# Kernel optimization log

Measured on AMD Instinct MI355X. Metric: run time of the kernel, lower is better.

Reference implementation:

```python
import jax, jax.numpy as jnp
import numpy as np

N_NODES = 100000
N_EDGES = 6_400_000
IN_DIM = 128


def gcn_conv(x, W, b, row, col, ew):
    """PyG GCNConv(normalize=True, add_self_loops=True) forward."""
    n = x.shape[0]
    loop = jnp.arange(n)
    row_sl = jnp.concatenate([row, loop])
    col_sl = jnp.concatenate([col, loop])
    ew_sl = jnp.concatenate([ew, jnp.ones((n,), ew.dtype)])
    # symmetric normalization: deg^{-1/2}[src] * w * deg^{-1/2}[dst]
    deg = jax.ops.segment_sum(ew_sl, col_sl, num_segments=n)
    safe_deg = jnp.where(deg > 0, deg, 1.0)
    dis = jnp.where(deg > 0, jax.lax.rsqrt(safe_deg), 0.0)
    norm = dis[row_sl] * ew_sl * dis[col_sl]
    h = x @ W  # [n, out_dim] linear transform first (small out_dim)
    # gather source features, scale, scatter-add into targets
    out = jax.ops.segment_sum(norm[:, None] * h[row_sl], col_sl, num_segments=n)
    return out + b


def setup_inputs() -> dict:
    key = jax.random.key(0)
    ks = jax.random.split(key, 12)
    X = jax.random.normal(ks[0], (N_NODES, IN_DIM), dtype=jnp.float32)
    edge_index = jax.random.randint(ks[1], (2, N_EDGES), 0, N_NODES, dtype=jnp.int64)
    edge_weight = jax.random.uniform(ks[2], (N_EDGES,), dtype=jnp.float32)

    def glorot(k, fan_in, fan_out):
        lim = np.sqrt(6.0 / (fan_in + fan_out)).astype(np.float32)
        return jax.random.uniform(k, (fan_in, fan_out), minval=-lim, maxval=lim, dtype=jnp.float32)

    return {
        "X": X,
        "edge_index": edge_index,
        "edge_weight": edge_weight,
        "W1": glorot(ks[3], IN_DIM, 12), "b1": jnp.zeros((12,), jnp.float32),
        "W2": glorot(ks[4], 12, 6), "b2": jnp.zeros((6,), jnp.float32),
        "W3": glorot(ks[5], 6, 3), "b3": jnp.zeros((3,), jnp.float32),
        "Wl": glorot(ks[6], 3, 1), "bl": jnp.zeros((1,), jnp.float32),
    }


def reference(X, edge_index, edge_weight, W1, b1, W2, b2, W3, b3, Wl, bl):
    row, col = edge_index[0], edge_index[1]
    h = jax.nn.relu(gcn_conv(X, W1, b1, row, col, edge_weight))
    # dropout p=0.2 is identity in eval mode
    h = jax.nn.relu(gcn_conv(h, W2, b2, row, col, edge_weight))
    h = jax.nn.relu(gcn_conv(h, W3, b3, row, col, edge_weight))
    out = jax.nn.sigmoid(h @ Wl + bl)
    return out.squeeze(1)  # [N]
```

## Files before the change

### kernel.cpp

```cpp
#include <hip/hip_runtime.h>
#include <cstdint>
#include <cstddef>

#define RANGE    128
#define RSHIFT   7
#define MAXBUCK  800
#define CSHIFT   12
#define CRANGE   4096
#define MAXC     32
#define FPB      32
#define CH_CNT   8192
#define CH_SC    4096
#define EPT      16
#define PAD      16
#define WSTR     132
#define STAGE_CAP 9216
#define KMAX     18

typedef _Float16 h8 __attribute__((ext_vector_type(8)));

__global__ void zero_pad_kernel(int* __restrict__ p, int n) {
    int i = blockIdx.x * blockDim.x + threadIdx.x;
    if (i < n) p[i * PAD] = 0;
}

__global__ void count_kernel(const int* __restrict__ col, int* __restrict__ fcnt,
                             int nfine, int E) {
    __shared__ int lcnt[MAXBUCK];
    int tid = threadIdx.x;
    for (int i = tid; i < nfine; i += blockDim.x) lcnt[i] = 0;
    __syncthreads();
    int base = blockIdx.x * CH_CNT;
    int end  = min(E, base + CH_CNT);
    for (int e = base + tid; e < end; e += blockDim.x)
        atomicAdd(&lcnt[col[e] >> RSHIFT], 1);
    __syncthreads();
    for (int i = tid; i < nfine; i += blockDim.x)
        if (lcnt[i]) atomicAdd(&fcnt[i * PAD], lcnt[i]);
}

__global__ void scan_kernel(const int* __restrict__ fcnt, int* __restrict__ fbase,
                            int* __restrict__ fcur, int* __restrict__ cbase,
                            int* __restrict__ ccur, int* __restrict__ row_ptr,
                            int nfine, int ncoarse, int N, int E) {
    __shared__ int lds[1024];
    int T = threadIdx.x;
    int s = (T < nfine) ? fcnt[T * PAD] : 0;
    lds[T] = s;
    __syncthreads();
    for (int off = 1; off < 1024; off <<= 1) {
        int v = (T >= off) ? lds[T - off] : 0;
        __syncthreads();
        lds[T] += v;
        __syncthreads();
    }
    int excl = lds[T] - s;
    if (T < nfine) { fbase[T] = excl; fcur[T * PAD] = excl; }
    if ((T & (FPB - 1)) == 0 && (T >> 5) < ncoarse) {
        cbase[T >> 5] = excl;
        ccur[(T >> 5) * PAD] = excl;
    }
    if (T == 0) { fbase[nfine] = E; cbase[ncoarse] = E; row_ptr[N] = E; }
}

__global__ void coarse_scatter_kernel(const int* __restrict__ row, const int* __restrict__ col,
                                      const float* __restrict__ ew, int* __restrict__ ccur,
                                      uint2* __restrict__ partA, int ncoarse, int E) {
    __shared__ uint2 stage[CH_SC];
    __shared__ unsigned char sb[CH_SC];
    __shared__ int lcnt[MAXC], lofs[MAXC], gofs[MAXC];
    __shared__ int total_s;
    int tid = threadIdx.x;
    if (tid < MAXC) lcnt[tid] = 0;
    __syncthreads();
    int base = blockIdx.x * CH_SC;
    int cnt  = min(E - base, CH_SC);

    uint2 rec[EPT]; int rnk[EPT]; int bb[EPT];
#pragma unroll
    for (int k = 0; k < EPT; k++) {
        int idx = tid + (k << 8);
        if (idx < cnt) {
            int e = base + idx;
            int c = col[e];
            int b = c >> CSHIFT;
            bb[k]  = b;
            rec[k] = make_uint2((unsigned)row[e] | ((unsigned)(c & (CRANGE - 1)) << 17),
                                __float_as_uint(ew[e]));
            rnk[k] = atomicAdd(&lcnt[b], 1);
        }
    }
    __syncthreads();
    if (tid == 0) {
        int run = 0;
        for (int i = 0; i < ncoarse; i++) { lofs[i] = run; run += lcnt[i]; }
        total_s = run;
    }
    __syncthreads();
    if (tid < ncoarse) {
        int c = lcnt[tid];
        if (c) {
            int g = atomicAdd(&ccur[tid * PAD], c);
            gofs[tid] = g - lofs[tid];
        }
    }
#pragma unroll
    for (int k = 0; k < EPT; k++) {
        int idx = tid + (k << 8);
        if (idx < cnt) {
            int p = lofs[bb[k]] + rnk[k];
            stage[p] = rec[k];
            sb[p] = (unsigned char)bb[k];
        }
    }
    __syncthreads();
    int total = total_s;
    for (int i = tid; i < total; i += 256)
        partA[gofs[sb[i]] + i] = stage[i];
}

__global__ __launch_bounds__(256, 3)
void fine_scatter_kernel(const uint2* __restrict__ partA, const int* __restrict__ cbase,
                                    int* __restrict__ fcur, uint2* __restrict__ partB,
                                    int nfine, int ncoarse, int E) {
    __shared__ uint2 stage[CH_SC];
    __shared__ unsigned short sb[CH_SC];
    __shared__ int lcnt[MAXBUCK], lofs[MAXBUCK], gofs[MAXBUCK];
    __shared__ int tmp[256];
    __shared__ int scb[MAXC + 1];
    __shared__ int rlo_s, total_s;
    int tid = threadIdx.x;
    int base = blockIdx.x * CH_SC;
    int cnt  = min(E - base, CH_SC);
    if (tid <= ncoarse) scb[tid] = cbase[tid];
    for (int i = tid; i < nfine; i += 256) lcnt[i] = 0;
    if (tid == 0) {
        int r = 0;
        while (r < ncoarse - 1 && cbase[r + 1] <= base) ++r;
        rlo_s = r;
    }
    __syncthreads();
    int rlo = rlo_s;

    uint2 rec[EPT]; int rnk[EPT]; int ff[EPT];
#pragma unroll
    for (int k = 0; k < EPT; k++) {
        int idx = tid + (k << 8);
        if (idx < cnt) {
            int e = base + idx;
            uint2 v = partA[e];
            int r = rlo;
            while (e >= scb[r + 1]) ++r;
            int col12 = (int)((v.x >> 17) & (CRANGE - 1));
            int f = (r << 5) | (col12 >> RSHIFT);
            ff[k]  = f;
            rec[k] = make_uint2((v.x & 0x1FFFFu) | ((unsigned)(col12 & (RANGE - 1)) << 17), v.y);
            rnk[k] = atomicAdd(&lcnt[f], 1);
        }
    }
    __syncthreads();
    {
        const int Cc = (nfine + 255) >> 8;
        int b0 = tid * Cc;
        int s = 0;
        for (int i = 0; i < Cc; i++) {
            int idx = b0 + i;
            if (idx < nfine) s += lcnt[idx];
        }
        tmp[tid] = s;
        __syncthreads();
        for (int off = 1; off < 256; off <<= 1) {
            int v = (tid >= off) ? tmp[tid - off] : 0;
            __syncthreads();
            tmp[tid] += v;
            __syncthreads();
        }
        int run = tmp[tid] - s;
        for (int i = 0; i < Cc; i++) {
            int idx = b0 + i;
            if (idx < nfine) { lofs[idx] = run; run += lcnt[idx]; }
        }
        if (tid == 255) total_s = tmp[255];
    }
    __syncthreads();
    for (int i = tid; i < nfine; i += 256) {
        int c = lcnt[i];
        if (c) {
            int g = atomicAdd(&fcur[i * PAD], c);
            gofs[i] = g - lofs[i];
        }
    }
#pragma unroll
    for (int k = 0; k < EPT; k++) {
        int idx = tid + (k << 8);
        if (idx < cnt) {
            int p = lofs[ff[k]] + rnk[k];
            stage[p] = rec[k];
            sb[p] = (unsigned short)ff[k];
        }
    }
    __syncthreads();
    int total = total_s;
    for (int i = tid; i < total; i += 256)
        partB[gofs[sb[i]] + i] = stage[i];
}

__global__ __launch_bounds__(512, 4)
void bucket_csr_kernel(const uint2* __restrict__ part, const int* __restrict__ bbase,
                       int* __restrict__ row_ptr, float* __restrict__ dis,
                       uint2* __restrict__ csr, int N) {
    extern __shared__ uint2 stage[];
    __shared__ int   scnt[RANGE];
    __shared__ int   sscan[RANGE];
    __shared__ float sdeg[RANGE];
    __shared__ float sdis[RANGE];
    int b = blockIdx.x, tid = threadIdx.x;
    int s = bbase[b], t = bbase[b + 1];
    int cnt = t - s;
    if (tid < RANGE) { scnt[tid] = 0; sdeg[tid] = 1.0f; }
    __syncthreads();
    for (int idx = tid; idx < cnt; idx += 512) {
        uint2 r = part[s + idx];
        if (idx < STAGE_CAP) stage[idx] = r;
        int c = (r.x >> 17) & (RANGE - 1);
        atomicAdd(&scnt[c], 1);
        atomicAdd(&sdeg[c], __uint_as_float(r.y));
    }
    __syncthreads();
    int cnt_t = 0;
    if (tid < RANGE) { cnt_t = scnt[tid]; sscan[tid] = cnt_t; }
    __syncthreads();
    for (int off = 1; off < RANGE; off <<= 1) {
        int v = 0;
        if (tid < RANGE && tid >= off) v = sscan[tid - off];
        __syncthreads();
        if (tid < RANGE) sscan[tid] += v;
        __syncthreads();
    }
    if (tid < RANGE) {
        int excl = sscan[tid] - cnt_t;
        int node = b * RANGE + tid;
        float dn = rsqrtf(sdeg[tid]);
        sdis[tid] = dn;
        if (node < N) {
            row_ptr[node] = s + excl;
            dis[node] = dn;
        }
        scnt[tid] = excl;
    }
    __syncthreads();

    if (cnt <= STAGE_CAP) {
        uint2 rc[KMAX]; int rp[KMAX];
#pragma unroll
        for (int k = 0; k < KMAX; k++) {
            int idx = tid + k * 512;
            if (idx < cnt) {
                uint2 r = stage[idx];
                int c   = (r.x >> 17) & (RANGE - 1);
                float v = sdis[c] * __uint_as_float(r.y);
                rp[k] = atomicAdd(&scnt[c], 1);
                rc[k] = make_uint2(r.x & 0x1FFFFu, __float_as_uint(v));
            }
        }
        __syncthreads();
#pragma unroll
        for (int k = 0; k < KMAX; k++) {
            int idx = tid + k * 512;
            if (idx < cnt) stage[rp[k]] = rc[k];
        }
        __syncthreads();
        for (int i = tid; i < cnt; i += 512)
            csr[s + i] = stage[i];
    } else {
        for (int idx = tid; idx < cnt; idx += 512) {
            uint2 r = (idx < STAGE_CAP) ? stage[idx] : part[s + idx];
            int c   = (r.x >> 17) & (RANGE - 1);
            float v = sdis[c] * __uint_as_float(r.y);
            int off = atomicAdd(&scnt[c], 1);
            csr[s + off] = make_uint2(r.x & 0x1FFFFu, __float_as_uint(v));
        }
    }
}

__global__ void lin1_kernel(const float* __restrict__ X, const float* __restrict__ W1,
                            const float* __restrict__ dis, uint4* __restrict__ t1, int n) {
    __shared__ float w1t[12 * WSTR];
    int tid = threadIdx.x;
    for (int i = tid; i < 128 * 12; i += 256) {
        int k = i / 12, o = i - k * 12;
        w1t[o * WSTR + k] = W1[i];
    }
    __syncthreads();
    int gt   = blockIdx.x * 256 + tid;
    int node = gt >> 3;
    int sub  = gt & 7;
    if (node >= n) return;

    const float4* xp = (const float4*)(X + (size_t)node * 128 + sub * 16);
    float4 x0 = xp[0], x1 = xp[1], x2 = xp[2], x3 = xp[3];

    float res[12];
#pragma unroll
    for (int o = 0; o < 12; o++) {
        const float4* wp = (const float4*)(w1t + o * WSTR + sub * 16);
        float4 w0 = wp[0], w1v = wp[1], w2 = wp[2], w3 = wp[3];
        float s;
        s  = x0.x * w0.x + x0.y * w0.y + x0.z * w0.z + x0.w * w0.w;
        s += x1.x * w1v.x + x1.y * w1v.y + x1.z * w1v.z + x1.w * w1v.w;
        s += x2.x * w2.x + x2.y * w2.y + x2.z * w2.z + x2.w * w2.w;
        s += x3.x * w3.x + x3.y * w3.y + x3.z * w3.z + x3.w * w3.w;
        res[o] = s;
    }
#pragma unroll
    for (int o = 0; o < 12; o++) {
        res[o] += __shfl_xor(res[o], 1, 64);
        res[o] += __shfl_xor(res[o], 2, 64);
        res[o] += __shfl_xor(res[o], 4, 64);
    }
    if (sub == 0) {
        h8 a, b;
#pragma unroll
        for (int o = 0; o < 8; o++) a[o] = (_Float16)res[o];
#pragma unroll
        for (int o = 0; o < 4; o++) b[o] = (_Float16)res[8 + o];
#pragma unroll
        for (int o = 4; o < 8; o++) b[o] = (_Float16)0.f;
        uint4 ua = __builtin_bit_cast(uint4, a);
        uint4 ub = __builtin_bit_cast(uint4, b);
        ub.z = __float_as_uint(dis[node]);
        ub.w = 0u;
        uint4* dst = t1 + (size_t)node * 2;
        dst[0] = ua;
        dst[1] = ub;
    }
}

template <int DIN, int ROWW, int DOUT, bool LAST>
__global__ void agg_kernel(const int* __restrict__ row_ptr, const uint2* __restrict__ csr,
                           const uint4* __restrict__ hin,
                           const float* __restrict__ b_this, const float* __restrict__ W_next,
                           const float* __restrict__ b_next, void* __restrict__ hout_v, int n) {
    int gt   = blockIdx.x * blockDim.x + threadIdx.x;
    int node = gt >> 3;
    int sub  = gt & 7;
    if (node >= n) return;
    int start = row_ptr[node];
    int end   = row_ptr[node + 1];
    float acc[DIN], acc2[DIN];
#pragma unroll
    for (int d = 0; d < DIN; d++) { acc[d] = 0.f; acc2[d] = 0.f; }

    auto body = [&](unsigned long long raw, float* a_) {
        int src    = (int)(unsigned)raw;
        float ewdd = __uint_as_float((unsigned)(raw >> 32));
        const uint4* hr = hin + (size_t)src * ROWW;
        if constexpr (DIN == 12) {
            uint4 ua = hr[0], ub = hr[1];
            float norm = ewdd * __uint_as_float(ub.z);
            h8 a = __builtin_bit_cast(h8, ua);
            h8 b = __builtin_bit_cast(h8, ub);
#pragma unroll
            for (int d = 0; d < 8; d++) a_[d] += norm * (float)a[d];
#pragma unroll
            for (int d = 0; d < 4; d++) a_[8 + d] += norm * (float)b[d];
        } else if constexpr (DIN == 6) {
            uint4 u = hr[0];
            float norm = ewdd * __uint_as_float(u.w);
            h8 a = __builtin_bit_cast(h8, u);
#pragma unroll
            for (int d = 0; d < 6; d++) a_[d] += norm * (float)a[d];
        } else {
            uint4 u = hr[0];
            float norm = ewdd * __uint_as_float(u.z);
            h8 a = __builtin_bit_cast(h8, u);
#pragma unroll
            for (int d = 0; d < 3; d++) a_[d] += norm * (float)a[d];
        }
    };

    int e = start + sub;
    for (; e + 8 < end; e += 16) {
        unsigned long long raw0 =
            __builtin_nontemporal_load((const unsigned long long*)(csr + e));
        unsigned long long raw1 =
            __builtin_nontemporal_load((const unsigned long long*)(csr + e + 8));
        body(raw0, acc);
        body(raw1, acc2);
    }
    if (e < end) {
        unsigned long long raw0 =
            __builtin_nontemporal_load((const unsigned long long*)(csr + e));
        body(raw0, acc);
    }

#pragma unroll
    for (int d = 0; d < DIN; d++) {
        acc[d] += acc2[d];
        acc[d] += __shfl_xor(acc[d], 1, 64);
        acc[d] += __shfl_xor(acc[d], 2, 64);
        acc[d] += __shfl_xor(acc[d], 4, 64);
    }

    if (sub == 0) {
        const uint4* hn = hin + (size_t)node * ROWW;
        float v[DIN];
        float dn;
        if constexpr (DIN == 12) {
            uint4 ua = hn[0], ub = hn[1];
            dn = __uint_as_float(ub.z);
            float s2 = dn * dn;
            h8 a = __builtin_bit_cast(h8, ua);
            h8 b = __builtin_bit_cast(h8, ub);
#pragma unroll
            for (int d = 0; d < 8; d++) v[d] = fmaxf(acc[d] + s2 * (float)a[d] + b_this[d], 0.f);
#pragma unroll
            for (int d = 0; d < 4; d++) v[8 + d] = fmaxf(acc[8 + d] + s2 * (float)b[d] + b_this[8 + d], 0.f);
        } else if constexpr (DIN == 6) {
            uint4 u = hn[0];
            dn = __uint_as_float(u.w);
            float s2 = dn * dn;
            h8 a = __builtin_bit_cast(h8, u);
#pragma unroll
            for (int d = 0; d < 6; d++) v[d] = fmaxf(acc[d] + s2 * (float)a[d] + b_this[d], 0.f);
        } else {
            uint4 u = hn[0];
            dn = __uint_as_float(u.z);
            float s2 = dn * dn;
            h8 a = __builtin_bit_cast(h8, u);
#pragma unroll
            for (int d = 0; d < 3; d++) v[d] = fmaxf(acc[d] + s2 * (float)a[d] + b_this[d], 0.f);
        }
        if constexpr (!LAST) {
            float o[DOUT];
#pragma unroll
            for (int oo = 0; oo < DOUT; oo++) {
                float z = 0.f;
#pragma unroll
                for (int d = 0; d < DIN; d++) z += v[d] * W_next[d * DOUT + oo];
                o[oo] = z;
            }
            h8 w;
#pragma unroll
            for (int oo = 0; oo < 8; oo++) w[oo] = (_Float16)0.f;
#pragma unroll
            for (int oo = 0; oo < DOUT; oo++) w[oo] = (_Float16)o[oo];
            uint4 uw = __builtin_bit_cast(uint4, w);
            if constexpr (DOUT == 6) uw.w = __float_as_uint(dn);
            else                     uw.z = __float_as_uint(dn);
            ((uint4*)hout_v)[node] = uw;
        } else {
            float z = b_next[0];
#pragma unroll
            for (int d = 0; d < DIN; d++) z += v[d] * W_next[d];
            ((float*)hout_v)[node] = 1.0f / (1.0f + expf(-z));
        }
    }
}

extern "C" void kernel_launch(void* const* d_in, const int* in_sizes, int n_in,
                              void* d_out, int out_size, void* d_ws, size_t ws_size,
                              hipStream_t stream) {
    const float* X  = (const float*)d_in[0];
    const int*   ei = (const int*)d_in[1];
    const float* ew = (const float*)d_in[2];
    const float* W1 = (const float*)d_in[3];
    const float* b1 = (const float*)d_in[4];
    const float* W2 = (const float*)d_in[5];
    const float* b2 = (const float*)d_in[6];
    const float* W3 = (const float*)d_in[7];
    const float* b3 = (const float*)d_in[8];
    const float* Wl = (const float*)d_in[9];
    const float* bl = (const float*)d_in[10];
    float* out = (float*)d_out;

    const int N = in_sizes[0] / 128;
    const int E = in_sizes[1] / 2;
    const int* row = ei;
    const int* col = ei + E;
    const int nfine   = (N + RANGE - 1) >> RSHIFT;
    const int ncoarse = (N + CRANGE - 1) >> CSHIFT;

    char* ws = (char*)d_ws;
    size_t off = 0;
    auto carve = [&](size_t bytes) -> void* {
        void* p = ws + off;
        off += (bytes + 255) & ~(size_t)255;
        return p;
    };
    int*   fcnt    = (int*)  carve((size_t)MAXBUCK * PAD * 4);
    int*   fcur    = (int*)  carve((size_t)MAXBUCK * PAD * 4);
    int*   ccur    = (int*)  carve((size_t)MAXC * PAD * 4);
    int*   cbase   = (int*)  carve((size_t)(MAXC + 1) * 4);
    int*   fbase   = (int*)  carve((size_t)(MAXBUCK + 1) * 4);
    int*   row_ptr = (int*)  carve((size_t)(N + 1) * 4);
    float* dis     = (float*)carve((size_t)N * 4);
    uint2* partA   = (uint2*)carve((size_t)E * 8);
    uint2* partB   = (uint2*)carve((size_t)E * 8);
    uint2* csr = partA;
    uint4* t1  = (uint4*)partB;
    uint4* t2  = t1 + (size_t)N * 2;
    uint4* t3  = t2 + (size_t)N;
    (void)ws_size; (void)n_in; (void)out_size;

    const int bCnt = (E + CH_CNT - 1) / CH_CNT;
    const int bSc  = (E + CH_SC - 1) / CH_SC;
    const int bL   = ((size_t)N * 8 + 255) / 256;
    const int bA   = ((size_t)N * 8 + 255) / 256;

    zero_pad_kernel<<<(nfine + 255) / 256, 256, 0, stream>>>(fcnt, nfine);
    count_kernel<<<bCnt, 256, 0, stream>>>(col, fcnt, nfine, E);
    scan_kernel<<<1, 1024, 0, stream>>>(fcnt, fbase, fcur, cbase, ccur, row_ptr,
                                        nfine, ncoarse, N, E);
    coarse_scatter_kernel<<<bSc, 256, 0, stream>>>(row, col, ew, ccur, partA, ncoarse, E);
    fine_scatter_kernel<<<bSc, 256, 0, stream>>>(partA, cbase, fcur, partB, nfine, ncoarse, E);
    bucket_csr_kernel<<<nfine, 512, (size_t)STAGE_CAP * sizeof(uint2), stream>>>(
        partB, fbase, row_ptr, dis, csr, N);
    lin1_kernel<<<bL, 256, 0, stream>>>(X, W1, dis, t1, N);
    agg_kernel<12, 2, 6, false><<<bA, 256, 0, stream>>>(row_ptr, csr, t1, b1, W2, nullptr, t2, N);
    agg_kernel< 6, 1, 3, false><<<bA, 256, 0, stream>>>(row_ptr, csr, t2, b2, W3, nullptr, t3, N);
    agg_kernel< 3, 1, 1, true ><<<bA, 256, 0, stream>>>(row_ptr, csr, t3, b3, Wl, bl, out, N);
}
```

Before: 515.7 us.

## Stage CSR segments into LDS via async global_load_lds in bucket and agg kernels

Uses the AMD global_load_lds builtin to copy each block's contiguous CSR/partition records straight into shared memory, in bucket_csr_kernel and in the three aggregation kernels. Each aggregation block now covers 32 nodes, loads their edge range (up to 3072 records) into LDS, then has threads read edges from LDS, falling back to global reads when the range overflows. The copies may read past the segment end, so the partB allocation is padded. This adds LDS pressure and a full wait plus barrier before compute, which may reduce occupancy and overlap.

```diff
diff --git a/kernel.cpp b/kernel.cpp
--- a/kernel.cpp
+++ b/kernel.cpp
@@ -16,8 +16,14 @@
 #define WSTR     132
 #define STAGE_CAP 9216
 #define KMAX     18
+#define SCAP     3072
 
 typedef _Float16 h8 __attribute__((ext_vector_type(8)));
+
+#define GLOAD_LDS16(gsrc, ldsb)                                                   \
+    __builtin_amdgcn_global_load_lds(                                             \
+        (const __attribute__((address_space(1))) uint32_t*)(gsrc),                \
+        (__attribute__((address_space(3))) uint32_t*)(ldsb), 16, 0, 0)
 
 __global__ void zero_pad_kernel(int* __restrict__ p, int n) {
     int i = blockIdx.x * blockDim.x + threadIdx.x;
@@ -217,11 +223,27 @@
     int b = blockIdx.x, tid = threadIdx.x;
     int s = bbase[b], t = bbase[b + 1];
     int cnt = t - s;
+    int lim = min(cnt, STAGE_CAP);
     if (tid < RANGE) { scnt[tid] = 0; sdeg[tid] = 1.0f; }
-    __syncthreads();
-    for (int idx = tid; idx < cnt; idx += 512) {
+    {
+        int wave = tid >> 6, lane = tid & 63;
+        int iters = (lim + 1023) >> 10;
+        for (int it = 0; it < iters; ++it) {
+            int recBase = (it << 10) + (wave << 7);
+            const uint2* src = part + s + recBase + (lane << 1);
+            GLOAD_LDS16(src, (char*)stage + ((size_t)recBase << 3));
+        }
+    }
+    asm volatile("s_waitcnt vmcnt(0)" ::: "memory");
+    __syncthreads();
+    for (int idx = tid; idx < lim; idx += 512) {
+        uint2 r = stage[idx];
+        int c = (r.x >> 17) & (RANGE - 1);
+        atomicAdd(&scnt[c], 1);
+        atomicAdd(&sdeg[c], __uint_as_float(r.y));
+    }
+    for (int idx = STAGE_CAP + tid; idx < cnt; idx += 512) {
         uint2 r = part[s + idx];
-        if (idx < STAGE_CAP) stage[idx] = r;
         int c = (r.x >> 17) & (RANGE - 1);
         atomicAdd(&scnt[c], 1);
         atomicAdd(&sdeg[c], __uint_as_float(r.y));
@@ -337,13 +359,33 @@
 }
 
 template <int DIN, int ROWW, int DOUT, bool LAST>
-__global__ void agg_kernel(const int* __restrict__ row_ptr, const uint2* __restrict__ csr,
-                           const uint4* __restrict__ hin,
-                           const float* __restrict__ b_this, const float* __restrict__ W_next,
-                           const float* __restrict__ b_next, void* __restrict__ hout_v, int n) {
-    int gt   = blockIdx.x * blockDim.x + threadIdx.x;
-    int node = gt >> 3;
-    int sub  = gt & 7;
+__global__ __launch_bounds__(256)
+void agg_kernel(const int* __restrict__ row_ptr, const uint2* __restrict__ csr,
+                const uint4* __restrict__ hin,
+                const float* __restrict__ b_this, const float* __restrict__ W_next,
+                const float* __restrict__ b_next, void* __restrict__ hout_v, int n) {
+    __shared__ uint2 scsr[SCAP];
+    int tid = threadIdx.x;
+    int nodeBase = blockIdx.x << 5;
+    int node = nodeBase + (tid >> 3);
+    int sub  = tid & 7;
+    int endNode  = min(nodeBase + 32, n);
+    int blkStart = row_ptr[nodeBase];
+    int blkEnd   = row_ptr[endNode];
+    int blkCnt   = blkEnd - blkStart;
+    int lim = min(blkCnt, SCAP);
+    {
+        int wave = tid >> 6, lane = tid & 63;
+        int iters = (lim + 511) >> 9;
+        for (int it = 0; it < iters; ++it) {
+            int recBase = (it << 9) + (wave << 7);
+            const uint2* src = csr + blkStart + recBase + (lane << 1);
+            GLOAD_LDS16(src, (char*)scsr + ((size_t)recBase << 3));
+        }
+    }
+    asm volatile("s_waitcnt vmcnt(0)" ::: "memory");
+    __syncthreads();
+
     if (node >= n) return;
     int start = row_ptr[node];
     int end   = row_ptr[node + 1];
@@ -351,9 +393,9 @@
 #pragma unroll
     for (int d = 0; d < DIN; d++) { acc[d] = 0.f; acc2[d] = 0.f; }
 
-    auto body = [&](unsigned long long raw, float* a_) {
-        int src    = (int)(unsigned)raw;
-        float ewdd = __uint_as_float((unsigned)(raw >> 32));
+    auto body = [&](uint2 r, float* a_) {
+        int src    = (int)(r.x);
+        float ewdd = __uint_as_float(r.y);
         const uint4* hr = hin + (size_t)src * ROWW;
         if constexpr (DIN == 12) {
             uint4 ua = hr[0], ub = hr[1];
@@ -379,19 +421,26 @@
         }
     };
 
-    int e = start + sub;
-    for (; e + 8 < end; e += 16) {
-        unsigned long long raw0 =
-            __builtin_nontemporal_load((const unsigned long long*)(csr + e));
-        unsigned long long raw1 =
-            __builtin_nontemporal_load((const unsigned long long*)(csr + e + 8));
-        body(raw0, acc);
-        body(raw1, acc2);
-    }
-    if (e < end) {
-        unsigned long long raw0 =
-            __builtin_nontemporal_load((const unsigned long long*)(csr + e));
-        body(raw0, acc);
+    if (blkCnt <= SCAP) {
+        int ls = start - blkStart;
+        int le = end - blkStart;
+        int e = ls + sub;
+        for (; e + 8 < le; e += 16) {
+            uint2 r0 = scsr[e];
+            uint2 r1 = scsr[e + 8];
+            body(r0, acc);
+            body(r1, acc2);
+        }
+        if (e < le) body(scsr[e], acc);
+    } else {
+        int e = start + sub;
+        for (; e + 8 < end; e += 16) {
+            uint2 r0 = csr[e];
+            uint2 r1 = csr[e + 8];
+            body(r0, acc);
+            body(r1, acc2);
+        }
+        if (e < end) body(csr[e], acc);
     }
 
 #pragma unroll
@@ -496,7 +545,7 @@
     int*   row_ptr = (int*)  carve((size_t)(N + 1) * 4);
     float* dis     = (float*)carve((size_t)N * 4);
     uint2* partA   = (uint2*)carve((size_t)E * 8);
-    uint2* partB   = (uint2*)carve((size_t)E * 8);
+    uint2* partB   = (uint2*)carve((size_t)(E + 1024) * 8);
     uint2* csr = partA;
     uint4* t1  = (uint4*)partB;
     uint4* t2  = t1 + (size_t)N * 2;
@@ -506,7 +555,7 @@
     const int bCnt = (E + CH_CNT - 1) / CH_CNT;
     const int bSc  = (E + CH_SC - 1) / CH_SC;
     const int bL   = ((size_t)N * 8 + 255) / 256;
-    const int bA   = ((size_t)N * 8 + 255) / 256;
+    const int bA   = (N + 31) / 32;
 
     zero_pad_kernel<<<(nfine + 255) / 256, 256, 0, stream>>>(fcnt, nfine);
     count_kernel<<<bCnt, 256, 0, stream>>>(col, fcnt, nfine, E);
```

Result: faster. 466.5 us (-9.6%).
